# Performance work log

Measured on AMD Instinct MI355X. Metric: run time of the kernel, lower is better.

Reference implementation:

```python
import jax, jax.numpy as jnp
import numpy as np

MU = jnp.array([1.0, 0.9, 0.7, 0.5, 0.3, 0.1, -0.1, -0.3, -0.5, -0.7, -0.9], dtype=jnp.float32)
SIGMA = jnp.array([1e-3] + [0.1] * 10, dtype=jnp.float32)
H = 8  # n_head


def _lin(x, W, b):
    return x @ W.T + b


def _knrm_logsum(eq, ed, mq, md):
    # eq:[B,Q,D] ed:[B,L,D] mq:[B,Q] md:[B,L] -> [B,K]
    qn = eq / jnp.maximum(jnp.linalg.norm(eq, axis=2, keepdims=True), 1e-12)
    dn = ed / jnp.maximum(jnp.linalg.norm(ed, axis=2, keepdims=True), 1e-12)
    sim = jnp.einsum('bqe,bde->bqd', qn, dn)
    pv = jnp.exp(-(sim[..., None] - MU) ** 2 / (2.0 * SIGMA ** 2))  # [B,Q,L,K]
    ps = jnp.sum(pv * md[:, None, :, None], axis=2)                 # [B,Q,K]
    lps = jnp.log(jnp.clip(ps, 1e-10, None)) * mq[..., None] * 0.01
    return jnp.sum(lps, axis=1)


def _mha(x, Wq, bq, Wk, bk, Wv, bv, Wo, bo):
    # CyberZHG-style MultiHeadAttention: relu on q/k/v projections and output.
    B, L, D = x.shape
    dh = D // H

    def split(t):
        return t.reshape(B, L, H, dh).transpose(0, 2, 1, 3)

    q = split(jax.nn.relu(_lin(x, Wq, bq)))
    k = split(jax.nn.relu(_lin(x, Wk, bk)))
    v = split(jax.nn.relu(_lin(x, Wv, bv)))
    att = jax.nn.softmax(jnp.einsum('bhqe,bhke->bhqk', q, k) / jnp.sqrt(jnp.float32(dh)), axis=-1)
    y = jnp.einsum('bhqk,bhke->bhqe', att, v).transpose(0, 2, 1, 3).reshape(B, L, D)
    return jax.nn.relu(_lin(y, Wo, bo))


def _forward(masks_q, masks_d, masks_dcq, masks_dbody, emb, Wq, bq, Wk, bk, Wv, bv, Wo, bo,
             tW, tb, qdW, qdb, qbW, qbb, qcqW, qcqb, dcqW, dcqb, bcqW, bcqb,
             expW, expb, combW, combb, inputs_q, inputs_d, inputs_dcq, inputs_dbody):
    eq = emb[inputs_q]
    ed = emb[inputs_d]
    eb = emb[inputs_dbody]
    qd = jnp.tanh(_lin(_knrm_logsum(eq, ed, masks_q, masks_d), qdW, qdb))
    qb = jnp.tanh(_lin(_knrm_logsum(eq, eb, masks_q, masks_dbody), qbW, qbb))
    B, MN, ML = inputs_dcq.shape
    e_dcq = jax.nn.relu(_lin(emb[inputs_dcq.reshape(B, MN * ML)], tW, tb))
    enc_dcq = _mha(e_dcq, Wq, bq, Wk, bk, Wv, bv, Wo, bo).reshape(B, MN, ML, -1)
    enc_d = _mha(ed, Wq, bq, Wk, bk, Wv, bv, Wo, bo)
    enc_b = _mha(eb, Wq, bq, Wk, bk, Wv, bv, Wo, bo)

    def per_cq(i_dcq, m_dcq):  # i_dcq:[B,ML,D] m_dcq:[B,ML]
        return (_knrm_logsum(eq, i_dcq, masks_q, m_dcq),
                _knrm_logsum(enc_d, i_dcq, masks_d, m_dcq),
                _knrm_logsum(enc_b, i_dcq, masks_dbody, m_dcq))

    kq, kd, kb = jax.vmap(per_cq, in_axes=(1, 1))(enc_dcq, masks_dcq)  # [MN,B,K]
    qcqres = jnp.tanh(_lin(kq, qcqW, qcqb))      # [MN,B,1]
    qcqdattn = jnp.tanh(_lin(kd, dcqW, dcqb))
    qcqbattn = jnp.tanh(_lin(kb, bcqW, bcqb))
    qcqd = jnp.sum(qcqres * qcqdattn, axis=0)    # [B,1]
    qcqb2 = jnp.sum(qcqres * qcqbattn, axis=0)
    qcq = _lin(jnp.concatenate([qcqd, qcqb2], axis=1), expW, expb)
    return jnp.tanh(_lin(jnp.concatenate([qd, qb, qcq], axis=1), combW, combb)).squeeze()


def setup_inputs():
    B, Q, DL, BL, MN, ML, D, V = 32, 20, 64, 512, 8, 16, 128, 50000
    key = jax.random.key(0)
    ks = jax.random.split(key, 40)

    def w(i, shape, s=0.05):
        return jax.random.normal(ks[i], shape, jnp.float32) * s

    return {
        'inputs_q': jax.random.randint(ks[0], (B, Q), 1, V),
        'inputs_d': jax.random.randint(ks[1], (B, DL), 1, V),
        'inputs_dcq': jax.random.randint(ks[2], (B, MN, ML), 1, V),
        'inputs_dbody': jax.random.randint(ks[3], (B, BL), 1, V),
        'masks_q': jnp.ones((B, Q), jnp.float32),
        'masks_d': jnp.ones((B, DL), jnp.float32),
        'masks_dcq': jnp.ones((B, MN, ML), jnp.float32),
        'masks_dbody': jnp.ones((B, BL), jnp.float32),
        'emb': w(4, (V, D), 0.1).at[0].set(0.0),  # padding_idx=0
        'Wq': w(5, (D, D)), 'bq': w(6, (D,)),
        'Wk': w(7, (D, D)), 'bk': w(8, (D,)),
        'Wv': w(9, (D, D)), 'bv': w(10, (D,)),
        'Wo': w(11, (D, D)), 'bo': w(12, (D,)),
        'tW': w(13, (D, D)), 'tb': w(14, (D,)),
        'qdW': w(15, (1, 11)), 'qdb': w(16, (1,)),
        'qbW': w(17, (1, 11)), 'qbb': w(18, (1,)),
        'qcqW': w(19, (1, 11)), 'qcqb': w(20, (1,)),
        'dcqW': w(21, (1, 11)), 'dcqb': w(22, (1,)),
        'bcqW': w(23, (1, 11)), 'bcqb': w(24, (1,)),
        'expW': w(25, (1, 2)), 'expb': w(26, (1,)),
        'combW': w(27, (1, 3)), 'combb': w(28, (1,)),
    }


def reference(inputs_q, inputs_d, inputs_dcq, inputs_dbody, masks_q, masks_d, masks_dcq, masks_dbody,
              emb, Wq, bq, Wk, bk, Wv, bv, Wo, bo, tW, tb, qdW, qdb, qbW, qbb, qcqW, qcqb,
              dcqW, dcqb, bcqW, bcqb, expW, expb, combW, combb):
    return _forward(masks_q, masks_d, masks_dcq, masks_dbody, emb, Wq, bq, Wk, bk, Wv, bv, Wo, bo,
                    tW, tb, qdW, qdb, qbW, qbb, qcqW, qcqb, dcqW, dcqb, bcqW, bcqb,
                    expW, expb, combW, combb, inputs_q, inputs_d, inputs_dcq, inputs_dbody)
```

## Files before the change

### kernel.cpp

```cpp
#include <hip/hip_runtime.h>
#include <hip/hip_bf16.h>

#define BB 32
#define QL_ 20
#define DL_ 64
#define BL_ 512
#define MN_ 8
#define ML_ 16
#define DD 128
#define HH 8

#define ROWS_DCQ 4096
#define ROWS_D   2048
#define ROWS_B   16384
#define R_ALL    22528
#define ROWS_EQ  640
#define R_GATHER 23168

typedef float f2 __attribute__((ext_vector_type(2)));

__global__ __launch_bounds__(256) void gather_all(
    const int* __restrict__ in_q, const int* __restrict__ in_d,
    const int* __restrict__ in_dcq, const int* __restrict__ in_db,
    const float* __restrict__ emb, float* __restrict__ x_all, float* __restrict__ ytmp,
    float* __restrict__ inv_eq, float* __restrict__ inv_ed, float* __restrict__ inv_eb,
    float* __restrict__ zero_p, int nzero) {
    int blk = blockIdx.x;
    if (blk >= 2896) {
        int i = (blk - 2896) * 256 + threadIdx.x;
        if (i < nzero) zero_p[i] = 0.f;
        return;
    }
    int t = blk * 256 + threadIdx.x;
    int r = t >> 5, c = t & 31;
    const int* idx; float* outp; float* invp; int lr;
    if (r < ROWS_DCQ)              { idx = in_dcq; outp = ytmp + (size_t)r * DD;  invp = nullptr; lr = r; }
    else if (r < ROWS_DCQ + ROWS_D){ idx = in_d;   outp = x_all + (size_t)r * DD; invp = inv_ed;  lr = r - ROWS_DCQ; }
    else if (r < R_ALL)            { idx = in_db;  outp = x_all + (size_t)r * DD; invp = inv_eb;  lr = r - (ROWS_DCQ + ROWS_D); }
    else                           { idx = in_q;   outp = x_all + (size_t)r * DD; invp = inv_eq;  lr = r - R_ALL; }
    float4 val = ((const float4*)(emb + (size_t)idx[lr] * DD))[c];
    ((float4*)outp)[c] = val;
    float ss = val.x * val.x + val.y * val.y + val.z * val.z + val.w * val.w;
    ss += __shfl_xor(ss, 1, 64);
    ss += __shfl_xor(ss, 2, 64);
    ss += __shfl_xor(ss, 4, 64);
    ss += __shfl_xor(ss, 8, 64);
    ss += __shfl_xor(ss, 16, 64);
    if (c == 0 && invp) invp[lr] = 1.0f / fmaxf(sqrtf(ss), 1e-12f);
}

__device__ __forceinline__ void linear_body(float* __restrict__ wT, float* __restrict__ bs,
                                            const float* __restrict__ in, const float* __restrict__ W,
                                            const float* __restrict__ bias, float* __restrict__ out,
                                            float* __restrict__ inv_out, int block) {
    int t = threadIdx.x;
    for (int i = t; i < DD * DD; i += 256) {
        int o = i >> 7, e = i & 127;
        wT[e * 132 + o] = W[i];
    }
    if (t < 128) bs[t] = bias[t];
    __syncthreads();
    int og = t & 15, rg = t >> 4;
    int rowbase = block * 128 + rg * 8;
    f2 acc[8][4];
#pragma unroll
    for (int r = 0; r < 8; r++)
#pragma unroll
        for (int p = 0; p < 4; p++) acc[r][p] = f2{0.f, 0.f};
    for (int e4 = 0; e4 < 32; e4++) {
        float4 xv[8];
#pragma unroll
        for (int r = 0; r < 8; r++)
            xv[r] = *(const float4*)&in[(size_t)(rowbase + r) * DD + 4 * e4];
#pragma unroll
        for (int ee = 0; ee < 4; ee++) {
            int e = 4 * e4 + ee;
            float4 wa = *(const float4*)&wT[e * 132 + 8 * og];
            float4 wb = *(const float4*)&wT[e * 132 + 8 * og + 4];
            f2 w0 = {wa.x, wa.y}, w1 = {wa.z, wa.w}, w2 = {wb.x, wb.y}, w3 = {wb.z, wb.w};
#pragma unroll
            for (int r = 0; r < 8; r++) {
                float x = ((const float*)&xv[r])[ee];
                f2 x2 = {x, x};
                acc[r][0] = __builtin_elementwise_fma(x2, w0, acc[r][0]);
                acc[r][1] = __builtin_elementwise_fma(x2, w1, acc[r][1]);
                acc[r][2] = __builtin_elementwise_fma(x2, w2, acc[r][2]);
                acc[r][3] = __builtin_elementwise_fma(x2, w3, acc[r][3]);
            }
        }
    }
    float4 ba = *(const float4*)&bs[8 * og];
    float4 bbv = *(const float4*)&bs[8 * og + 4];
    float ss[8];
#pragma unroll
    for (int r = 0; r < 8; r++) {
        float o0 = fmaxf(acc[r][0].x + ba.x, 0.f);
        float o1 = fmaxf(acc[r][0].y + ba.y, 0.f);
        float o2 = fmaxf(acc[r][1].x + ba.z, 0.f);
        float o3 = fmaxf(acc[r][1].y + ba.w, 0.f);
        float o4 = fmaxf(acc[r][2].x + bbv.x, 0.f);
        float o5 = fmaxf(acc[r][2].y + bbv.y, 0.f);
        float o6 = fmaxf(acc[r][3].x + bbv.z, 0.f);
        float o7 = fmaxf(acc[r][3].y + bbv.w, 0.f);
        float4 s1 = {o0, o1, o2, o3}, s2 = {o4, o5, o6, o7};
        float* op = out + (size_t)(rowbase + r) * DD + 8 * og;
        *(float4*)op = s1;
        *(float4*)(op + 4) = s2;
        ss[r] = o0 * o0 + o1 * o1 + o2 * o2 + o3 * o3 + o4 * o4 + o5 * o5 + o6 * o6 + o7 * o7;
    }
    if (inv_out) {
#pragma unroll
        for (int r = 0; r < 8; r++) {
            ss[r] += __shfl_xor(ss[r], 1, 64);
            ss[r] += __shfl_xor(ss[r], 2, 64);
            ss[r] += __shfl_xor(ss[r], 4, 64);
            ss[r] += __shfl_xor(ss[r], 8, 64);
        }
#pragma unroll
        for (int r = 0; r < 8; r++)
            if (og == r) inv_out[rowbase + r] = 1.0f / fmaxf(sqrtf(ss[r]), 1e-12f);
    }
}

__global__ __launch_bounds__(256) void lin_kernel(const float* __restrict__ in, const float* __restrict__ W,
                                                  const float* __restrict__ bias, float* __restrict__ out,
                                                  float* __restrict__ inv_out) {
    __shared__ float wT[DD * 132];
    __shared__ float bs[DD];
    linear_body(wT, bs, in, W, bias, out, inv_out, blockIdx.x);
}

__global__ __launch_bounds__(256) void qkv_all(const float* __restrict__ x,
                                               const float* __restrict__ Wq, const float* __restrict__ bq,
                                               const float* __restrict__ Wk, const float* __restrict__ bk,
                                               const float* __restrict__ Wv, const float* __restrict__ bv,
                                               float* __restrict__ q, float* __restrict__ k, float* __restrict__ v) {
    __shared__ float wT[DD * 132];
    __shared__ float bs[DD];
    int sel = blockIdx.x / 176, blk = blockIdx.x % 176;
    const float* W = (sel == 0) ? Wq : (sel == 1) ? Wk : Wv;
    const float* B = (sel == 0) ? bq : (sel == 1) ? bk : bv;
    float* O = (sel == 0) ? q : (sel == 1) ? k : v;
    linear_body(wT, bs, x, W, B, O, nullptr, blk);
}

__device__ __forceinline__ void attn512_v5(float* __restrict__ sm,
                                           const float* __restrict__ q, const float* __restrict__ k,
                                           const float* __restrict__ v, float* __restrict__ y, int bh) {
    float* ks = sm;
    float* vs = sm + 512 * 16;
    int h = bh & 7, b = bh >> 3;
    int t = threadIdx.x;
    const size_t base = (size_t)b * 512 * DD + h * 16;
    for (int i = t; i < 512 * 4; i += 1024) {
        int j = i >> 2, c = i & 3;
        *(float4*)&ks[j * 16 + 4 * c] = *(const float4*)&k[base + (size_t)j * DD + 4 * c];
        *(float4*)&vs[j * 16 + 4 * c] = *(const float4*)&v[base + (size_t)j * DD + 4 * c];
    }
    int w = t >> 6, lane = t & 63;
    int kg = w & 3, qw = w >> 2;
    int r0 = qw * 128 + lane;
    const float* qp0 = q + base + (size_t)r0 * DD;
    const float* qp1 = qp0 + 64 * DD;
    float qA[16], qB[16];
#pragma unroll
    for (int c = 0; c < 4; c++) {
        *(float4*)&qA[4 * c] = *(const float4*)(qp0 + 4 * c);
        *(float4*)&qB[4 * c] = *(const float4*)(qp1 + 4 * c);
    }
    f2 qv[16];
#pragma unroll
    for (int e = 0; e < 16; e++) qv[e] = f2{qA[e] * 0.25f, qB[e] * 0.25f};
    f2 acc[16];
    f2 l2 = {0.f, 0.f};
#pragma unroll
    for (int e = 0; e < 16; e++) acc[e] = f2{0.f, 0.f};
    __syncthreads();
    int j0 = kg * 128;
    for (int j = j0; j < j0 + 128; j++) {
        float kk[16], vv[16];
#pragma unroll
        for (int c = 0; c < 4; c++) {
            *(float4*)&kk[4 * c] = *(const float4*)&ks[j * 16 + 4 * c];
            *(float4*)&vv[4 * c] = *(const float4*)&vs[j * 16 + 4 * c];
        }
        f2 s0 = qv[0] * f2{kk[0], kk[0]};
        f2 s1 = qv[1] * f2{kk[1], kk[1]};
        f2 s2 = qv[2] * f2{kk[2], kk[2]};
        f2 s3 = qv[3] * f2{kk[3], kk[3]};
#pragma unroll
        for (int e = 4; e < 16; e += 4) {
            s0 = __builtin_elementwise_fma(qv[e + 0], f2{kk[e + 0], kk[e + 0]}, s0);
            s1 = __builtin_elementwise_fma(qv[e + 1], f2{kk[e + 1], kk[e + 1]}, s1);
            s2 = __builtin_elementwise_fma(qv[e + 2], f2{kk[e + 2], kk[e + 2]}, s2);
            s3 = __builtin_elementwise_fma(qv[e + 3], f2{kk[e + 3], kk[e + 3]}, s3);
        }
        f2 d = (s0 + s1) + (s2 + s3);
        f2 p = {__expf(d.x), __expf(d.y)};
        l2 += p;
#pragma unroll
        for (int e = 0; e < 16; e++)
            acc[e] = __builtin_elementwise_fma(p, f2{vv[e], vv[e]}, acc[e]);
    }
    __syncthreads();
#pragma unroll
    for (int g = 1; g < 4; g++) {
        if (kg == g) {
            float* p0 = &sm[r0 * 17];
            float* p1 = &sm[(r0 + 64) * 17];
#pragma unroll
            for (int e = 0; e < 16; e++) { p0[e] = acc[e].x; p1[e] = acc[e].y; }
            p0[16] = l2.x;
            p1[16] = l2.y;
        }
        __syncthreads();
        if (kg == 0) {
            const float* p0 = &sm[r0 * 17];
            const float* p1 = &sm[(r0 + 64) * 17];
#pragma unroll
            for (int e = 0; e < 16; e++) { acc[e].x += p0[e]; acc[e].y += p1[e]; }
            l2.x += p0[16];
            l2.y += p1[16];
        }
        __syncthreads();
    }
    if (kg == 0) {
        float ix = 1.0f / l2.x, iy = 1.0f / l2.y;
        float o0[16], o1[16];
#pragma unroll
        for (int e = 0; e < 16; e++) { o0[e] = acc[e].x * ix; o1[e] = acc[e].y * iy; }
        float* yp0 = y + base + (size_t)r0 * DD;
        float* yp1 = yp0 + 64 * DD;
#pragma unroll
        for (int c = 0; c < 4; c++) {
            *(float4*)(yp0 + 4 * c) = *(const float4*)&o0[4 * c];
            *(float4*)(yp1 + 4 * c) = *(const float4*)&o1[4 * c];
        }
    }
}

template <int L, int NQ>
__device__ __forceinline__ void attn_body(float* __restrict__ sm, const float* __restrict__ q,
                                          const float* __restrict__ k, const float* __restrict__ v,
                                          float* __restrict__ y, int bh) {
    constexpr int WAVES = 16;
    constexpr int WQ = L / (32 * NQ);
    constexpr int KG = WAVES / WQ;
    constexpr int KPG = L / KG;
    float* ks = sm;
    float* vs = sm + L * 16;
    int h = bh & 7, b = bh >> 3;
    int t = threadIdx.x;
    const size_t base = (size_t)b * L * DD + h * 16;
    for (int i = t; i < L * 4; i += 1024) {
        int j = i >> 2, c = i & 3;
        *(float4*)&ks[j * 16 + 4 * c] = *(const float4*)&k[base + (size_t)j * DD + 4 * c];
        *(float4*)&vs[j * 16 + 4 * c] = *(const float4*)&v[base + (size_t)j * DD + 4 * c];
    }
    int w = t >> 6, lane = t & 63;
    int ls = lane & 31, eh = lane >> 5;
    int kg = w % KG, qw = w / KG;
    int qb2 = qw * 32 * NQ;
    f2 qv[NQ][4];
#pragma unroll
    for (int n = 0; n < NQ; n++) {
        int qr = qb2 + ls + 32 * n;
        const float* qp = q + base + (size_t)qr * DD + eh * 8;
        float4 a = *(const float4*)qp;
        float4 b4 = *(const float4*)(qp + 4);
        qv[n][0] = f2{a.x, a.y};   qv[n][1] = f2{a.z, a.w};
        qv[n][2] = f2{b4.x, b4.y}; qv[n][3] = f2{b4.z, b4.w};
    }
    f2 acc[NQ][4];
    float l[NQ];
#pragma unroll
    for (int n = 0; n < NQ; n++) {
#pragma unroll
        for (int m = 0; m < 4; m++) acc[n][m] = f2{0.f, 0.f};
        l[n] = 0.f;
    }
    __syncthreads();
    for (int j = kg * KPG; j < (kg + 1) * KPG; j++) {
        float4 ka = *(const float4*)&ks[j * 16 + eh * 8];
        float4 kb2 = *(const float4*)&ks[j * 16 + eh * 8 + 4];
        float4 va = *(const float4*)&vs[j * 16 + eh * 8];
        float4 vb2 = *(const float4*)&vs[j * 16 + eh * 8 + 4];
        f2 kk0 = {ka.x, ka.y}, kk1 = {ka.z, ka.w}, kk2 = {kb2.x, kb2.y}, kk3 = {kb2.z, kb2.w};
        f2 vv0 = {va.x, va.y}, vv1 = {va.z, va.w}, vv2 = {vb2.x, vb2.y}, vv3 = {vb2.z, vb2.w};
#pragma unroll
        for (int n = 0; n < NQ; n++) {
            f2 d2 = qv[n][0] * kk0;
            d2 = __builtin_elementwise_fma(qv[n][1], kk1, d2);
            d2 = __builtin_elementwise_fma(qv[n][2], kk2, d2);
            d2 = __builtin_elementwise_fma(qv[n][3], kk3, d2);
            float sh = d2.x + d2.y;
            float s = sh + __shfl_xor(sh, 32, 64);
            float p = __expf(s * 0.25f);
            l[n] += p;
            f2 p2 = {p, p};
            acc[n][0] = __builtin_elementwise_fma(p2, vv0, acc[n][0]);
            acc[n][1] = __builtin_elementwise_fma(p2, vv1, acc[n][1]);
            acc[n][2] = __builtin_elementwise_fma(p2, vv2, acc[n][2]);
            acc[n][3] = __builtin_elementwise_fma(p2, vv3, acc[n][3]);
        }
    }
    __syncthreads();
    if (kg > 0) {
#pragma unroll
        for (int n = 0; n < NQ; n++) {
            int qr = qb2 + ls + 32 * n;
            float* pp = &sm[((kg - 1) * L + qr) * 20 + eh * 10];
            *(f2*)&pp[0] = acc[n][0];
            *(f2*)&pp[2] = acc[n][1];
            *(f2*)&pp[4] = acc[n][2];
            *(f2*)&pp[6] = acc[n][3];
            pp[8] = l[n];
        }
    }
    __syncthreads();
    if (kg == 0) {
#pragma unroll
        for (int n = 0; n < NQ; n++) {
            int qr = qb2 + ls + 32 * n;
            f2 a0 = acc[n][0], a1 = acc[n][1], a2 = acc[n][2], a3 = acc[n][3];
            float lt = l[n];
#pragma unroll
            for (int g = 1; g < KG; g++) {
                const float* pp = &sm[((g - 1) * L + qr) * 20 + eh * 10];
                a0 += *(const f2*)&pp[0];
                a1 += *(const f2*)&pp[2];
                a2 += *(const f2*)&pp[4];
                a3 += *(const f2*)&pp[6];
                lt += pp[8];
            }
            float inv = 1.0f / lt;
            float4 o1 = {a0.x * inv, a0.y * inv, a1.x * inv, a1.y * inv};
            float4 o2 = {a2.x * inv, a2.y * inv, a3.x * inv, a3.y * inv};
            float* yp = y + base + (size_t)qr * DD + eh * 8;
            *(float4*)yp = o1;
            *(float4*)(yp + 4) = o2;
        }
    }
}

__global__ __launch_bounds__(1024) void attn_all(const float* __restrict__ qb_, const float* __restrict__ kb_,
                                                 const float* __restrict__ vb_, float* __restrict__ yb_) {
    __shared__ float sm[16384];
    int blk = blockIdx.x;
    if (blk < 256) {
        const size_t off = (size_t)(ROWS_DCQ + ROWS_D) * DD;
        attn512_v5(sm, qb_ + off, kb_ + off, vb_ + off, yb_ + off, blk);
    } else if (blk < 512) {
        attn_body<128, 1>(sm, qb_, kb_, vb_, yb_, blk - 256);
    } else {
        const size_t off = (size_t)ROWS_DCQ * DD;
        attn_body<64, 1>(sm, qb_ + off, kb_ + off, vb_ + off, yb_ + off, blk - 512);
    }
}

template <int QPT, int DPT>
__device__ void knrm_core(float* __restrict__ sm,
                          const float* __restrict__ Q, const float* __restrict__ invQ,
                          const float* __restrict__ mq, int QL, int q0, int qbase,
                          const float* __restrict__ D, const float* __restrict__ invD,
                          const float* __restrict__ md, int DL, int dbase, int mdbase,
                          float* __restrict__ out) {
    constexpr int QT = QPT * 16, DT = DPT * 16;
    float* qtile = sm;
    float* dtile = qtile + QT * 132;
    float* mdv = dtile + DT * 132;
    float* red = mdv + DT;
    float* outred = red + 4 * 16 * QPT * 11;
    const float MUc[11] = {1.0f, 0.9f, 0.7f, 0.5f, 0.3f, 0.1f, -0.1f, -0.3f, -0.5f, -0.7f, -0.9f};
    const float NC[11]  = {-500000.0f, -50.f, -50.f, -50.f, -50.f, -50.f, -50.f, -50.f, -50.f, -50.f, -50.f};
    int t = threadIdx.x;
    int tq = t & 15, td = t >> 4;
    if (t < 11) outred[t] = 0.f;
    for (int i = t; i < QT * 32; i += 256) {
        int r = i >> 5, c = i & 31;
        int qrow = q0 + r;
        float4 val = make_float4(0.f, 0.f, 0.f, 0.f);
        if (qrow < QL) {
            float s = invQ[qbase + qrow];
            float4 g = *(const float4*)(Q + (size_t)(qbase + qrow) * DD + 4 * c);
            val = make_float4(g.x * s, g.y * s, g.z * s, g.w * s);
        }
        *(float4*)&qtile[r * 132 + 4 * c] = val;
    }
    float ps[QPT][11];
#pragma unroll
    for (int i = 0; i < QPT; i++)
#pragma unroll
        for (int kk = 0; kk < 11; kk++) ps[i][kk] = 0.f;

    for (int d0 = 0; d0 < DL; d0 += DT) {
        for (int i = t; i < DT * 32; i += 256) {
            int r = i >> 5, c = i & 31;
            int drow = d0 + r;
            float4 val = make_float4(0.f, 0.f, 0.f, 0.f);
            if (drow < DL) {
                float s = invD[dbase + drow];
                float4 g = *(const float4*)(D + (size_t)(dbase + drow) * DD + 4 * c);
                val = make_float4(g.x * s, g.y * s, g.z * s, g.w * s);
            }
            *(float4*)&dtile[r * 132 + 4 * c] = val;
        }
        if (t < DT) mdv[t] = (d0 + t < DL) ? md[mdbase + d0 + t] : 0.f;
        __syncthreads();
        float dot[QPT][DPT];
#pragma unroll
        for (int i = 0; i < QPT; i++)
#pragma unroll
            for (int j = 0; j < DPT; j++) dot[i][j] = 0.f;
#pragma unroll 2
        for (int e4 = 0; e4 < 32; e4++) {
            float4 qv[QPT], dv[DPT];
#pragma unroll
            for (int i = 0; i < QPT; i++) qv[i] = *(const float4*)&qtile[(tq + 16 * i) * 132 + 4 * e4];
#pragma unroll
            for (int j = 0; j < DPT; j++) dv[j] = *(const float4*)&dtile[(td + 16 * j) * 132 + 4 * e4];
#pragma unroll
            for (int i = 0; i < QPT; i++)
#pragma unroll
                for (int j = 0; j < DPT; j++)
                    dot[i][j] += qv[i].x * dv[j].x + qv[i].y * dv[j].y + qv[i].z * dv[j].z + qv[i].w * dv[j].w;
        }
#pragma unroll
        for (int j = 0; j < DPT; j++) {
            float m = mdv[td + 16 * j];
#pragma unroll
            for (int i = 0; i < QPT; i++) {
                float sim = dot[i][j];
#pragma unroll
                for (int kk = 0; kk < 11; kk++) {
                    float df = sim - MUc[kk];
                    ps[i][kk] = fmaf(__expf(df * df * NC[kk]), m, ps[i][kk]);
                }
            }
        }
        __syncthreads();
    }
#pragma unroll
    for (int i = 0; i < QPT; i++)
#pragma unroll
        for (int kk = 0; kk < 11; kk++) {
            ps[i][kk] += __shfl_xor(ps[i][kk], 16, 64);
            ps[i][kk] += __shfl_xor(ps[i][kk], 32, 64);
        }
    int w = t >> 6;
    if ((t & 63) < 16) {
#pragma unroll
        for (int i = 0; i < QPT; i++)
#pragma unroll
            for (int kk = 0; kk < 11; kk++) red[(w * 16 + tq) * (QPT * 11) + i * 11 + kk] = ps[i][kk];
    }
    __syncthreads();
    for (int i = t; i < 16 * QPT * 11; i += 256) {
        int tq2 = i / (QPT * 11);
        int rem = i - tq2 * (QPT * 11);
        int qi = rem / 11, kk = rem - qi * 11;
        float s = red[(0 * 16 + tq2) * (QPT * 11) + qi * 11 + kk] + red[(1 * 16 + tq2) * (QPT * 11) + qi * 11 + kk]
                + red[(2 * 16 + tq2) * (QPT * 11) + qi * 11 + kk] + red[(3 * 16 + tq2) * (QPT * 11) + qi * 11 + kk];
        int qrow = q0 + tq2 + 16 * qi;
        if (qrow < QL) {
            float lps = logf(fmaxf(s, 1e-10f)) * mq[qbase + qrow] * 0.01f;
            atomicAdd(&outred[kk], lps);
        }
    }
    __syncthreads();
    if (t < 11) atomicAdd(&out[t], outred[t]);
}

__global__ __launch_bounds__(256) void knrm_all(
    const float* __restrict__ eq, const float* __restrict__ inv_eq, const float* __restrict__ mask_q,
    const float* __restrict__ ed, const float* __restrict__ inv_ed, const float* __restrict__ mask_d,
    const float* __restrict__ eb, const float* __restrict__ inv_eb, const float* __restrict__ mask_db,
    const float* __restrict__ enc_d, const float* __restrict__ inv_encd,
    const float* __restrict__ enc_b, const float* __restrict__ inv_encb,
    const float* __restrict__ enc_dcq, const float* __restrict__ inv_encdcq, const float* __restrict__ mask_dcq,
    float* __restrict__ qdk, float* __restrict__ qbk,
    float* __restrict__ kq, float* __restrict__ kd, float* __restrict__ kb) {
    __shared__ float sm[14155];
    int blk = blockIdx.x;
    if (blk < 32) {
        int b = blk;
        knrm_core<2, 4>(sm, eq, inv_eq, mask_q, QL_, 0, b * QL_, ed, inv_ed, mask_d, DL_, b * DL_, b * DL_, qdk + b * 11);
    } else if (blk < 64) {
        int b = blk - 32;
        knrm_core<2, 4>(sm, eq, inv_eq, mask_q, QL_, 0, b * QL_, eb, inv_eb, mask_db, BL_, b * BL_, b * BL_, qbk + b * 11);
    } else {
        int u = blk - 64;
        int sub = u % 10;
        int ib = u / 10;
        int b = ib & 31, inst = ib >> 5;
        int dbase = b * (MN_ * ML_) + inst * ML_;
        if (sub == 0)
            knrm_core<4, 1>(sm, eq, inv_eq, mask_q, QL_, 0, b * QL_, enc_dcq, inv_encdcq, mask_dcq, ML_, dbase, dbase,
                            kq + (size_t)(inst * BB + b) * 11);
        else if (sub == 1)
            knrm_core<4, 1>(sm, enc_d, inv_encd, mask_d, DL_, 0, b * DL_, enc_dcq, inv_encdcq, mask_dcq, ML_, dbase, dbase,
                            kd + (size_t)(inst * BB + b) * 11);
        else
            knrm_core<4, 1>(sm, enc_b, inv_encb, mask_db, BL_, (sub - 2) * 64, b * BL_, enc_dcq, inv_encdcq, mask_dcq, ML_,
                            dbase, dbase, kb + (size_t)(inst * BB + b) * 11);
    }
}

__device__ inline float dot11(const float* w, const float* x) {
    float s = 0.f;
#pragma unroll
    for (int k = 0; k < 11; k++) s += w[k] * x[k];
    return s;
}

__global__ void final_kernel(const float* __restrict__ qdk, const float* __restrict__ qbk,
                             const float* __restrict__ kq, const float* __restrict__ kd,
                             const float* __restrict__ kb,
                             const float* qdW, const float* qdb, const float* qbW, const float* qbb,
                             const float* qcqW, const float* qcqb, const float* dcqW, const float* dcqb,
                             const float* bcqW, const float* bcqb, const float* expW, const float* expb,
                             const float* combW, const float* combb, float* __restrict__ out) {
    int b = threadIdx.x;
    if (b >= BB) return;
    float qd = tanhf(dot11(qdW, qdk + b * 11) + qdb[0]);
    float qb = tanhf(dot11(qbW, qbk + b * 11) + qbb[0]);
    float qcqd = 0.f, qcqb2 = 0.f;
    for (int i = 0; i < MN_; i++) {
        int base = (i * BB + b) * 11;
        float r  = tanhf(dot11(qcqW, kq + base) + qcqb[0]);
        float da = tanhf(dot11(dcqW, kd + base) + dcqb[0]);
        float ba = tanhf(dot11(bcqW, kb + base) + bcqb[0]);
        qcqd += r * da;
        qcqb2 += r * ba;
    }
    float qcq = expW[0] * qcqd + expW[1] * qcqb2 + expb[0];
    out[b] = tanhf(combW[0] * qd + combW[1] * qb + combW[2] * qcq + combb[0]);
}

extern "C" void kernel_launch(void* const* d_in, const int* in_sizes, int n_in,
                              void* d_out, int out_size, void* d_ws, size_t ws_size,
                              hipStream_t stream) {
    const int*   in_q    = (const int*)d_in[0];
    const int*   in_d    = (const int*)d_in[1];
    const int*   in_dcq  = (const int*)d_in[2];
    const int*   in_db   = (const int*)d_in[3];
    const float* mask_q  = (const float*)d_in[4];
    const float* mask_d  = (const float*)d_in[5];
    const float* mask_dcq= (const float*)d_in[6];
    const float* mask_db = (const float*)d_in[7];
    const float* emb     = (const float*)d_in[8];
    const float* Wq = (const float*)d_in[9];   const float* bq = (const float*)d_in[10];
    const float* Wk = (const float*)d_in[11];  const float* bk = (const float*)d_in[12];
    const float* Wv = (const float*)d_in[13];  const float* bv = (const float*)d_in[14];
    const float* Wo = (const float*)d_in[15];  const float* bo = (const float*)d_in[16];
    const float* tW = (const float*)d_in[17];  const float* tb = (const float*)d_in[18];
    const float* qdW = (const float*)d_in[19]; const float* qdb = (const float*)d_in[20];
    const float* qbW = (const float*)d_in[21]; const float* qbb = (const float*)d_in[22];
    const float* qcqW = (const float*)d_in[23];const float* qcqb = (const float*)d_in[24];
    const float* dcqW = (const float*)d_in[25];const float* dcqb = (const float*)d_in[26];
    const float* bcqW = (const float*)d_in[27];const float* bcqb = (const float*)d_in[28];
    const float* expW = (const float*)d_in[29];const float* expb = (const float*)d_in[30];
    const float* combW = (const float*)d_in[31];const float* combb = (const float*)d_in[32];
    float* out = (float*)d_out;

    float* ws = (float*)d_ws;
    size_t off = 0;
    auto alloc = [&](size_t n) { float* p = ws + off; off += n; return p; };
    float* x_all = alloc((size_t)R_GATHER * DD);
    float* qbuf  = alloc((size_t)R_ALL * DD);
    float* kbuf  = alloc((size_t)R_ALL * DD);
    float* vbuf  = alloc((size_t)R_ALL * DD);
    float* ybuf  = alloc((size_t)R_ALL * DD);
    float* inv_eq  = alloc(ROWS_EQ);
    float* inv_ed  = alloc(ROWS_D);
    float* inv_eb  = alloc(ROWS_B);
    float* inv_enc = alloc(R_ALL);
    float* qdk = alloc(BB * 11);
    float* qbk = alloc(BB * 11);
    float* kq  = alloc(MN_ * BB * 11);
    float* kd  = alloc(MN_ * BB * 11);
    float* kb  = alloc(MN_ * BB * 11);
    (void)ws_size; (void)in_sizes; (void)n_in; (void)out_size;

    const float* eq      = x_all + (size_t)R_ALL * DD;
    const float* ed      = x_all + (size_t)ROWS_DCQ * DD;
    const float* eb      = x_all + (size_t)(ROWS_DCQ + ROWS_D) * DD;
    float* enc_all = qbuf;
    const float* enc_dcq = enc_all;
    const float* enc_d   = enc_all + (size_t)ROWS_DCQ * DD;
    const float* enc_b   = enc_all + (size_t)(ROWS_DCQ + ROWS_D) * DD;
    const float* inv_encdcq = inv_enc;
    const float* inv_encd   = inv_enc + ROWS_DCQ;
    const float* inv_encb   = inv_enc + ROWS_DCQ + ROWS_D;

    gather_all<<<2932, 256, 0, stream>>>(in_q, in_d, in_dcq, in_db, emb,
                                         x_all, ybuf, inv_eq, inv_ed, inv_eb, qdk, 9152);
    lin_kernel<<<ROWS_DCQ / 128, 256, 0, stream>>>(ybuf, tW, tb, x_all, nullptr);
    qkv_all<<<3 * (R_ALL / 128), 256, 0, stream>>>(x_all, Wq, bq, Wk, bk, Wv, bv, qbuf, kbuf, vbuf);
    attn_all<<<768, 1024, 0, stream>>>(qbuf, kbuf, vbuf, ybuf);
    lin_kernel<<<R_ALL / 128, 256, 0, stream>>>(ybuf, Wo, bo, enc_all, inv_enc);
    knrm_all<<<2624, 256, 0, stream>>>(eq, inv_eq, mask_q, ed, inv_ed, mask_d, eb, inv_eb, mask_db,
                                       enc_d, inv_encd, enc_b, inv_encb, enc_dcq, inv_encdcq, mask_dcq,
                                       qdk, qbk, kq, kd, kb);
    final_kernel<<<1, 64, 0, stream>>>(qdk, qbk, kq, kd, kb,
                                       qdW, qdb, qbW, qbb, qcqW, qcqb, dcqW, dcqb,
                                       bcqW, bcqb, expW, expb, combW, combb, out);
}
```

Measured before the change: 385.1 us.

## Halve attention block size and register-block four queries per thread

The attention kernel now runs 512-thread blocks with two blocks per CU. In the 512-length path each thread handles four query rows instead of two, so every K/V row read from shared memory feeds twice as many FMAs. Block indices are remapped head-major, and the attention output is written in place over the query buffer, with the encoder output reusing the key buffer, which frees one full intermediate buffer. The cost is a larger register footprint per thread (about 128 live floats for queries and accumulators), which under the 512x2 launch bound may spill or lower occupancy.

```diff
diff --git a/kernel.cpp b/kernel.cpp
--- a/kernel.cpp
+++ b/kernel.cpp
@@ -144,37 +144,43 @@
     linear_body(wT, bs, x, W, B, O, nullptr, blk);
 }
 
-__device__ __forceinline__ void attn512_v5(float* __restrict__ sm,
+__device__ __forceinline__ void attn512_v6(float* __restrict__ sm,
                                            const float* __restrict__ q, const float* __restrict__ k,
-                                           const float* __restrict__ v, float* __restrict__ y, int bh) {
+                                           const float* __restrict__ v, float* __restrict__ y,
+                                           int b, int h) {
     float* ks = sm;
     float* vs = sm + 512 * 16;
-    int h = bh & 7, b = bh >> 3;
     int t = threadIdx.x;
     const size_t base = (size_t)b * 512 * DD + h * 16;
-    for (int i = t; i < 512 * 4; i += 1024) {
+    for (int i = t; i < 512 * 4; i += 512) {
         int j = i >> 2, c = i & 3;
         *(float4*)&ks[j * 16 + 4 * c] = *(const float4*)&k[base + (size_t)j * DD + 4 * c];
         *(float4*)&vs[j * 16 + 4 * c] = *(const float4*)&v[base + (size_t)j * DD + 4 * c];
     }
     int w = t >> 6, lane = t & 63;
     int kg = w & 3, qw = w >> 2;
-    int r0 = qw * 128 + lane;
-    const float* qp0 = q + base + (size_t)r0 * DD;
-    const float* qp1 = qp0 + 64 * DD;
-    float qA[16], qB[16];
-#pragma unroll
-    for (int c = 0; c < 4; c++) {
-        *(float4*)&qA[4 * c] = *(const float4*)(qp0 + 4 * c);
-        *(float4*)&qB[4 * c] = *(const float4*)(qp1 + 4 * c);
-    }
-    f2 qv[16];
-#pragma unroll
-    for (int e = 0; e < 16; e++) qv[e] = f2{qA[e] * 0.25f, qB[e] * 0.25f};
-    f2 acc[16];
-    f2 l2 = {0.f, 0.f};
-#pragma unroll
-    for (int e = 0; e < 16; e++) acc[e] = f2{0.f, 0.f};
+    int r0 = qw * 256 + lane;
+    f2 qv[2][16];
+#pragma unroll
+    for (int p = 0; p < 2; p++) {
+        const float* qa = q + base + (size_t)(r0 + p * 128) * DD;
+        const float* qb2 = qa + 64 * DD;
+#pragma unroll
+        for (int c = 0; c < 4; c++) {
+            float4 va = *(const float4*)(qa + 4 * c);
+            float4 vb = *(const float4*)(qb2 + 4 * c);
+            qv[p][4 * c + 0] = f2{va.x * 0.25f, vb.x * 0.25f};
+            qv[p][4 * c + 1] = f2{va.y * 0.25f, vb.y * 0.25f};
+            qv[p][4 * c + 2] = f2{va.z * 0.25f, vb.z * 0.25f};
+            qv[p][4 * c + 3] = f2{va.w * 0.25f, vb.w * 0.25f};
+        }
+    }
+    f2 acc[2][16];
+    f2 l2[2] = {f2{0.f, 0.f}, f2{0.f, 0.f}};
+#pragma unroll
+    for (int p = 0; p < 2; p++)
+#pragma unroll
+        for (int e = 0; e < 16; e++) acc[p][e] = f2{0.f, 0.f};
     __syncthreads();
     int j0 = kg * 128;
     for (int j = j0; j < j0 + 128; j++) {
@@ -184,57 +190,73 @@
             *(float4*)&kk[4 * c] = *(const float4*)&ks[j * 16 + 4 * c];
             *(float4*)&vv[4 * c] = *(const float4*)&vs[j * 16 + 4 * c];
         }
-        f2 s0 = qv[0] * f2{kk[0], kk[0]};
-        f2 s1 = qv[1] * f2{kk[1], kk[1]};
-        f2 s2 = qv[2] * f2{kk[2], kk[2]};
-        f2 s3 = qv[3] * f2{kk[3], kk[3]};
-#pragma unroll
-        for (int e = 4; e < 16; e += 4) {
-            s0 = __builtin_elementwise_fma(qv[e + 0], f2{kk[e + 0], kk[e + 0]}, s0);
-            s1 = __builtin_elementwise_fma(qv[e + 1], f2{kk[e + 1], kk[e + 1]}, s1);
-            s2 = __builtin_elementwise_fma(qv[e + 2], f2{kk[e + 2], kk[e + 2]}, s2);
-            s3 = __builtin_elementwise_fma(qv[e + 3], f2{kk[e + 3], kk[e + 3]}, s3);
-        }
-        f2 d = (s0 + s1) + (s2 + s3);
-        f2 p = {__expf(d.x), __expf(d.y)};
-        l2 += p;
-#pragma unroll
-        for (int e = 0; e < 16; e++)
-            acc[e] = __builtin_elementwise_fma(p, f2{vv[e], vv[e]}, acc[e]);
+        f2 d0a = qv[0][0] * f2{kk[0], kk[0]};
+        f2 d1a = qv[0][1] * f2{kk[1], kk[1]};
+        f2 d0b = qv[1][0] * f2{kk[0], kk[0]};
+        f2 d1b = qv[1][1] * f2{kk[1], kk[1]};
+#pragma unroll
+        for (int e = 2; e < 16; e += 2) {
+            d0a = __builtin_elementwise_fma(qv[0][e], f2{kk[e], kk[e]}, d0a);
+            d1a = __builtin_elementwise_fma(qv[0][e + 1], f2{kk[e + 1], kk[e + 1]}, d1a);
+            d0b = __builtin_elementwise_fma(qv[1][e], f2{kk[e], kk[e]}, d0b);
+            d1b = __builtin_elementwise_fma(qv[1][e + 1], f2{kk[e + 1], kk[e + 1]}, d1b);
+        }
+        f2 da = d0a + d1a, db = d0b + d1b;
+        f2 pa = {__expf(da.x), __expf(da.y)};
+        f2 pb = {__expf(db.x), __expf(db.y)};
+        l2[0] += pa;
+        l2[1] += pb;
+#pragma unroll
+        for (int e = 0; e < 16; e++) {
+            f2 ve = {vv[e], vv[e]};
+            acc[0][e] = __builtin_elementwise_fma(pa, ve, acc[0][e]);
+            acc[1][e] = __builtin_elementwise_fma(pb, ve, acc[1][e]);
+        }
     }
     __syncthreads();
 #pragma unroll
     for (int g = 1; g < 4; g++) {
         if (kg == g) {
-            float* p0 = &sm[r0 * 17];
-            float* p1 = &sm[(r0 + 64) * 17];
-#pragma unroll
-            for (int e = 0; e < 16; e++) { p0[e] = acc[e].x; p1[e] = acc[e].y; }
-            p0[16] = l2.x;
-            p1[16] = l2.y;
+#pragma unroll
+            for (int p = 0; p < 2; p++) {
+                int ra = r0 + p * 128;
+                float* pa = &sm[ra * 20];
+                float* pb = &sm[(ra + 64) * 20];
+#pragma unroll
+                for (int e = 0; e < 16; e++) { pa[e] = acc[p][e].x; pb[e] = acc[p][e].y; }
+                pa[16] = l2[p].x;
+                pb[16] = l2[p].y;
+            }
         }
         __syncthreads();
         if (kg == 0) {
-            const float* p0 = &sm[r0 * 17];
-            const float* p1 = &sm[(r0 + 64) * 17];
-#pragma unroll
-            for (int e = 0; e < 16; e++) { acc[e].x += p0[e]; acc[e].y += p1[e]; }
-            l2.x += p0[16];
-            l2.y += p1[16];
+#pragma unroll
+            for (int p = 0; p < 2; p++) {
+                int ra = r0 + p * 128;
+                const float* pa = &sm[ra * 20];
+                const float* pb = &sm[(ra + 64) * 20];
+#pragma unroll
+                for (int e = 0; e < 16; e++) { acc[p][e].x += pa[e]; acc[p][e].y += pb[e]; }
+                l2[p].x += pa[16];
+                l2[p].y += pb[16];
+            }
         }
         __syncthreads();
     }
     if (kg == 0) {
-        float ix = 1.0f / l2.x, iy = 1.0f / l2.y;
-        float o0[16], o1[16];
-#pragma unroll
-        for (int e = 0; e < 16; e++) { o0[e] = acc[e].x * ix; o1[e] = acc[e].y * iy; }
-        float* yp0 = y + base + (size_t)r0 * DD;
-        float* yp1 = yp0 + 64 * DD;
-#pragma unroll
-        for (int c = 0; c < 4; c++) {
-            *(float4*)(yp0 + 4 * c) = *(const float4*)&o0[4 * c];
-            *(float4*)(yp1 + 4 * c) = *(const float4*)&o1[4 * c];
+#pragma unroll
+        for (int p = 0; p < 2; p++) {
+            float ix = 1.0f / l2[p].x, iy = 1.0f / l2[p].y;
+            float o0[16], o1[16];
+#pragma unroll
+            for (int e = 0; e < 16; e++) { o0[e] = acc[p][e].x * ix; o1[e] = acc[p][e].y * iy; }
+            float* yp0 = y + base + (size_t)(r0 + p * 128) * DD;
+            float* yp1 = yp0 + 64 * DD;
+#pragma unroll
+            for (int c = 0; c < 4; c++) {
+                *(float4*)(yp0 + 4 * c) = *(const float4*)&o0[4 * c];
+                *(float4*)(yp1 + 4 * c) = *(const float4*)&o1[4 * c];
+            }
         }
     }
 }
@@ -242,17 +264,16 @@
 template <int L, int NQ>
 __device__ __forceinline__ void attn_body(float* __restrict__ sm, const float* __restrict__ q,
                                           const float* __restrict__ k, const float* __restrict__ v,
-                                          float* __restrict__ y, int bh) {
-    constexpr int WAVES = 16;
+                                          float* __restrict__ y, int b, int h) {
+    constexpr int WAVES = 8;
     constexpr int WQ = L / (32 * NQ);
     constexpr int KG = WAVES / WQ;
     constexpr int KPG = L / KG;
     float* ks = sm;
     float* vs = sm + L * 16;
-    int h = bh & 7, b = bh >> 3;
     int t = threadIdx.x;
     const size_t base = (size_t)b * L * DD + h * 16;
-    for (int i = t; i < L * 4; i += 1024) {
+    for (int i = t; i < L * 4; i += 512) {
         int j = i >> 2, c = i & 3;
         *(float4*)&ks[j * 16 + 4 * c] = *(const float4*)&k[base + (size_t)j * DD + 4 * c];
         *(float4*)&vs[j * 16 + 4 * c] = *(const float4*)&v[base + (size_t)j * DD + 4 * c];
@@ -343,18 +364,20 @@
     }
 }
 
-__global__ __launch_bounds__(1024) void attn_all(const float* __restrict__ qb_, const float* __restrict__ kb_,
-                                                 const float* __restrict__ vb_, float* __restrict__ yb_) {
+__global__ __launch_bounds__(512, 2) void attn_all(const float* __restrict__ qb_, const float* __restrict__ kb_,
+                                                   const float* __restrict__ vb_, float* __restrict__ yb_) {
     __shared__ float sm[16384];
     int blk = blockIdx.x;
     if (blk < 256) {
         const size_t off = (size_t)(ROWS_DCQ + ROWS_D) * DD;
-        attn512_v5(sm, qb_ + off, kb_ + off, vb_ + off, yb_ + off, blk);
+        attn512_v6(sm, qb_ + off, kb_ + off, vb_ + off, yb_ + off, blk & 31, blk >> 5);
     } else if (blk < 512) {
-        attn_body<128, 1>(sm, qb_, kb_, vb_, yb_, blk - 256);
+        int local = blk - 256;
+        attn_body<128, 1>(sm, qb_, kb_, vb_, yb_, local & 31, local >> 5);
     } else {
+        int local = blk - 512;
         const size_t off = (size_t)ROWS_DCQ * DD;
-        attn_body<64, 1>(sm, qb_ + off, kb_ + off, vb_ + off, yb_ + off, blk - 512);
+        attn_body<64, 1>(sm, qb_ + off, kb_ + off, vb_ + off, yb_ + off, local & 31, local >> 5);
     }
 }
 
@@ -570,7 +593,6 @@
     float* qbuf  = alloc((size_t)R_ALL * DD);
     float* kbuf  = alloc((size_t)R_ALL * DD);
     float* vbuf  = alloc((size_t)R_ALL * DD);
-    float* ybuf  = alloc((size_t)R_ALL * DD);
     float* inv_eq  = alloc(ROWS_EQ);
     float* inv_ed  = alloc(ROWS_D);
     float* inv_eb  = alloc(ROWS_B);
@@ -585,7 +607,7 @@
     const float* eq      = x_all + (size_t)R_ALL * DD;
     const float* ed      = x_all + (size_t)ROWS_DCQ * DD;
     const float* eb      = x_all + (size_t)(ROWS_DCQ + ROWS_D) * DD;
-    float* enc_all = qbuf;
+    float* enc_all = kbuf;
     const float* enc_dcq = enc_all;
     const float* enc_d   = enc_all + (size_t)ROWS_DCQ * DD;
     const float* enc_b   = enc_all + (size_t)(ROWS_DCQ + ROWS_D) * DD;
@@ -594,11 +616,11 @@
     const float* inv_encb   = inv_enc + ROWS_DCQ + ROWS_D;
 
     gather_all<<<2932, 256, 0, stream>>>(in_q, in_d, in_dcq, in_db, emb,
-                                         x_all, ybuf, inv_eq, inv_ed, inv_eb, qdk, 9152);
-    lin_kernel<<<ROWS_DCQ / 128, 256, 0, stream>>>(ybuf, tW, tb, x_all, nullptr);
+                                         x_all, kbuf, inv_eq, inv_ed, inv_eb, qdk, 9152);
+    lin_kernel<<<ROWS_DCQ / 128, 256, 0, stream>>>(kbuf, tW, tb, x_all, nullptr);
     qkv_all<<<3 * (R_ALL / 128), 256, 0, stream>>>(x_all, Wq, bq, Wk, bk, Wv, bv, qbuf, kbuf, vbuf);
-    attn_all<<<768, 1024, 0, stream>>>(qbuf, kbuf, vbuf, ybuf);
-    lin_kernel<<<R_ALL / 128, 256, 0, stream>>>(ybuf, Wo, bo, enc_all, inv_enc);
+    attn_all<<<768, 512, 0, stream>>>(qbuf, kbuf, vbuf, qbuf);
+    lin_kernel<<<R_ALL / 128, 256, 0, stream>>>(qbuf, Wo, bo, enc_all, inv_enc);
     knrm_all<<<2624, 256, 0, stream>>>(eq, inv_eq, mask_q, ed, inv_ed, mask_d, eb, inv_eb, mask_db,
                                        enc_d, inv_encd, enc_b, inv_encb, enc_dcq, inv_encdcq, mask_dcq,
                                        qdk, qbk, kq, kd, kb);
```

Result: faster. 375.8 us (-2.4%).
